# Kernel optimization log

Measured on AMD Instinct MI355X. Metric: run time of the kernel, lower is better.

The kernel has to match this reference:

```python
import jax, jax.numpy as jnp
import numpy as np

R = 0.8      # jet radius used to normalize pairwise distances
BETA = 1.0   # EMD angular exponent (matches beta=1.0 in emd()/emd_loss default)


def setup_inputs() -> dict:
    key = jax.random.key(0)
    k1, k2, k3, k4 = jax.random.split(key, 4)
    Ni, Nj, D = 6144, 6144, 2   # event points, shape-sample points, (eta, phi)
    M, K = 1024, 256            # batched simplex projection: rows x components
    y_i = jax.random.normal(k1, (Ni, D), dtype=jnp.float32)
    y_j = jax.random.normal(k2, (Nj, D), dtype=jnp.float32)
    x = jax.random.uniform(k3, (Ni, Nj), dtype=jnp.float32)
    x_ij = x / jnp.sum(x)       # transport plan normalized to unit total mass
    f = jax.random.normal(k4, (M, K), dtype=jnp.float32)
    return {"y_i": y_i, "y_j": y_j, "x_ij": x_ij, "f": f}


def _activate(f):
    # Euclidean projection of each row of f onto the probability simplex
    # (sort descending -> running threshold -> relu shift), as in activate().
    m, n = f.shape
    u = jnp.sort(f, axis=1)[:, ::-1]                                   # [m, n] descending
    v = (jnp.cumsum(u, axis=1) - 1.0) / jnp.arange(1, n + 1, dtype=f.dtype)
    rho = jnp.sum((u > v).astype(jnp.int32), axis=1) - 1               # [m]
    w = jnp.take_along_axis(v, rho[:, None], axis=1)                   # [m, 1]
    return jax.nn.relu(f - w)


def _emd_loss(y_i, y_j, x_ij):
    # theta_ij = sum_d | ((y_i - y_j) / R)^beta |  ; loss = sum theta_ij * x_ij
    diff = (y_i[:, None, :] - y_j[None, :, :]) / R                     # [Ni, Nj, D]
    theta = jnp.sum(jnp.abs(diff ** BETA), axis=-1)                    # [Ni, Nj]
    return jnp.sum(theta * x_ij)


def reference(y_i, y_j, x_ij, f):
    loss = _emd_loss(y_i, y_j, x_ij)   # scalar EMD-style transport loss
    z_proj = _activate(f)              # [M, K] simplex-projected weights
    return (loss, z_proj)
```

## Files before the change

### kernel.cpp

```cpp
#include <hip/hip_runtime.h>

#define NI 6144
#define NJ 6144
#define M_ROWS 1024
#define K_COLS 256
#define ROWS_PER_BLOCK 6
#define EMD_BLOCKS (NI / ROWS_PER_BLOCK)

__global__ __launch_bounds__(256) void emd_partial_kernel(
    const float* __restrict__ y_i, const float* __restrict__ y_j,
    const float* __restrict__ x, float* __restrict__ partial) {
  __shared__ float4 yjs[NJ / 2];
  const float4* yj4 = (const float4*)y_j;
  for (int t = threadIdx.x; t < NJ / 2; t += 256) yjs[t] = yj4[t];
  __syncthreads();

  float acc = 0.0f;
  const int row0 = blockIdx.x * ROWS_PER_BLOCK;
  for (int r = 0; r < ROWS_PER_BLOCK; ++r) {
    const int i = row0 + r;
    const float yi0 = y_i[2 * i];
    const float yi1 = y_i[2 * i + 1];
    const float4* xrow = (const float4*)(x + (size_t)i * NJ);
#pragma unroll
    for (int t = 0; t < NJ / 4 / 256; ++t) {
      const int idx = threadIdx.x + t * 256;
      const float4 xv = xrow[idx];
      const float4 ya = yjs[2 * idx];
      const float4 yb = yjs[2 * idx + 1];
      acc += xv.x * (fabsf(yi0 - ya.x) + fabsf(yi1 - ya.y));
      acc += xv.y * (fabsf(yi0 - ya.z) + fabsf(yi1 - ya.w));
      acc += xv.z * (fabsf(yi0 - yb.x) + fabsf(yi1 - yb.y));
      acc += xv.w * (fabsf(yi0 - yb.z) + fabsf(yi1 - yb.w));
    }
  }

  for (int off = 32; off > 0; off >>= 1) acc += __shfl_down(acc, off, 64);
  __shared__ float wsum[4];
  const int lane = threadIdx.x & 63;
  const int wid = threadIdx.x >> 6;
  if (lane == 0) wsum[wid] = acc;
  __syncthreads();
  if (threadIdx.x == 0)
    partial[blockIdx.x] = wsum[0] + wsum[1] + wsum[2] + wsum[3];
}

__global__ __launch_bounds__(256) void simplex_and_finish_kernel(
    const float* __restrict__ f, const float* __restrict__ partial,
    float* __restrict__ out) {
  const int tid = threadIdx.x;

  if (blockIdx.x == M_ROWS) {
    float acc = partial[tid] + partial[tid + 256] + partial[tid + 512] +
                partial[tid + 768];
    for (int off = 32; off > 0; off >>= 1) acc += __shfl_down(acc, off, 64);
    __shared__ float wsum[4];
    const int lane = tid & 63;
    const int wid = tid >> 6;
    if (lane == 0) wsum[wid] = acc;
    __syncthreads();
    if (tid == 0)
      out[0] = (wsum[0] + wsum[1] + wsum[2] + wsum[3]) * 1.25f;
    return;
  }

  const int row = blockIdx.x;
  const float fv = f[row * K_COLS + tid];

  __shared__ float s[K_COLS];
  __shared__ float c0[K_COLS];
  __shared__ float c1[K_COLS];
  __shared__ float vbuf[K_COLS];

  s[tid] = fv;
  __syncthreads();

  for (int k = 2; k <= K_COLS; k <<= 1) {
    for (int j = k >> 1; j > 0; j >>= 1) {
      const int ixj = tid ^ j;
      if (ixj > tid) {
        const float a = s[tid];
        const float b = s[ixj];
        const bool asc = ((tid & k) == 0);
        if ((a > b) == asc) {
          s[tid] = b;
          s[ixj] = a;
        }
      }
      __syncthreads();
    }
  }

  const float u = s[K_COLS - 1 - tid];
  c0[tid] = u;
  __syncthreads();
  float* src = c0;
  float* dst = c1;
  for (int off = 1; off < K_COLS; off <<= 1) {
    float v = src[tid];
    if (tid >= off) v += src[tid - off];
    dst[tid] = v;
    __syncthreads();
    float* tmp = src; src = dst; dst = tmp;
  }
  const float cs = src[tid];
  const float vt = (cs - 1.0f) / (float)(tid + 1);
  vbuf[tid] = vt;
  const int cnt = __syncthreads_count(u > vt);
  const float w = vbuf[cnt - 1];

  out[1 + row * K_COLS + tid] = fmaxf(fv - w, 0.0f);
}

extern "C" void kernel_launch(void* const* d_in, const int* in_sizes, int n_in,
                              void* d_out, int out_size, void* d_ws,
                              size_t ws_size, hipStream_t stream) {
  const float* y_i = (const float*)d_in[0];
  const float* y_j = (const float*)d_in[1];
  const float* x   = (const float*)d_in[2];
  const float* f   = (const float*)d_in[3];
  float* out = (float*)d_out;
  float* partial = (float*)d_ws;

  emd_partial_kernel<<<EMD_BLOCKS, 256, 0, stream>>>(y_i, y_j, x, partial);
  simplex_and_finish_kernel<<<M_ROWS + 1, 256, 0, stream>>>(f, partial, out);
}
```

Before: 235.2 us.

## Split y_j into component arrays, interleave rows per block, shuffle-based sort and scan

The EMD kernel now stores the eta and phi components of y_j in separate shared arrays. It processes 8 rows per block with the row loop inside the column loop, so each y_j load from shared memory is reused across all rows and several independent x loads are in flight at once. The simplex kernel replaces its shared-memory bitonic sort and Hillis-Steele scan with wavefront shuffles, using shared memory only for the cross-wave stages. This cuts barriers and LDS traffic but raises register pressure. The finishing reduction is adjusted to the new count of 768 partials.

```diff
diff --git a/kernel.cpp b/kernel.cpp
--- a/kernel.cpp
+++ b/kernel.cpp
@@ -4,34 +4,48 @@
 #define NJ 6144
 #define M_ROWS 1024
 #define K_COLS 256
-#define ROWS_PER_BLOCK 6
+#define ROWS_PER_BLOCK 8
 #define EMD_BLOCKS (NI / ROWS_PER_BLOCK)
 
 __global__ __launch_bounds__(256) void emd_partial_kernel(
     const float* __restrict__ y_i, const float* __restrict__ y_j,
     const float* __restrict__ x, float* __restrict__ partial) {
-  __shared__ float4 yjs[NJ / 2];
-  const float4* yj4 = (const float4*)y_j;
-  for (int t = threadIdx.x; t < NJ / 2; t += 256) yjs[t] = yj4[t];
+  __shared__ float4 yj0v[NJ / 4];
+  __shared__ float4 yj1v[NJ / 4];
+  {
+    const float4* yj4 = (const float4*)y_j;
+    float* s0 = (float*)yj0v;
+    float* s1 = (float*)yj1v;
+    for (int t = threadIdx.x; t < NJ / 2; t += 256) {
+      const float4 v = yj4[t];
+      s0[2 * t]     = v.x;  s1[2 * t]     = v.y;
+      s0[2 * t + 1] = v.z;  s1[2 * t + 1] = v.w;
+    }
+  }
   __syncthreads();
 
+  const int row0 = blockIdx.x * ROWS_PER_BLOCK;
+  float yi0[ROWS_PER_BLOCK], yi1[ROWS_PER_BLOCK];
+#pragma unroll
+  for (int r = 0; r < ROWS_PER_BLOCK; ++r) {
+    yi0[r] = y_i[2 * (row0 + r)];
+    yi1[r] = y_i[2 * (row0 + r) + 1];
+  }
+
   float acc = 0.0f;
-  const int row0 = blockIdx.x * ROWS_PER_BLOCK;
-  for (int r = 0; r < ROWS_PER_BLOCK; ++r) {
-    const int i = row0 + r;
-    const float yi0 = y_i[2 * i];
-    const float yi1 = y_i[2 * i + 1];
-    const float4* xrow = (const float4*)(x + (size_t)i * NJ);
 #pragma unroll
-    for (int t = 0; t < NJ / 4 / 256; ++t) {
-      const int idx = threadIdx.x + t * 256;
-      const float4 xv = xrow[idx];
-      const float4 ya = yjs[2 * idx];
-      const float4 yb = yjs[2 * idx + 1];
-      acc += xv.x * (fabsf(yi0 - ya.x) + fabsf(yi1 - ya.y));
-      acc += xv.y * (fabsf(yi0 - ya.z) + fabsf(yi1 - ya.w));
-      acc += xv.z * (fabsf(yi0 - yb.x) + fabsf(yi1 - yb.y));
-      acc += xv.w * (fabsf(yi0 - yb.z) + fabsf(yi1 - yb.w));
+  for (int t = 0; t < NJ / 4 / 256; ++t) {
+    const int idx = threadIdx.x + t * 256;
+    const float4 ya = yj0v[idx];
+    const float4 yb = yj1v[idx];
+#pragma unroll
+    for (int r = 0; r < ROWS_PER_BLOCK; ++r) {
+      const float4 xv =
+          ((const float4*)(x + (size_t)(row0 + r) * NJ))[idx];
+      acc += xv.x * (fabsf(yi0[r] - ya.x) + fabsf(yi1[r] - yb.x));
+      acc += xv.y * (fabsf(yi0[r] - ya.y) + fabsf(yi1[r] - yb.y));
+      acc += xv.z * (fabsf(yi0[r] - ya.z) + fabsf(yi1[r] - yb.z));
+      acc += xv.w * (fabsf(yi0[r] - ya.w) + fabsf(yi1[r] - yb.w));
     }
   }
 
@@ -49,65 +63,81 @@
     const float* __restrict__ f, const float* __restrict__ partial,
     float* __restrict__ out) {
   const int tid = threadIdx.x;
+  const int lane = tid & 63;
+  const int wid = tid >> 6;
+
+  __shared__ float s[K_COLS];
+  __shared__ float wpre[4];
 
   if (blockIdx.x == M_ROWS) {
-    float acc = partial[tid] + partial[tid + 256] + partial[tid + 512] +
-                partial[tid + 768];
+    float acc = partial[tid] + partial[tid + 256] + partial[tid + 512];
     for (int off = 32; off > 0; off >>= 1) acc += __shfl_down(acc, off, 64);
-    __shared__ float wsum[4];
-    const int lane = tid & 63;
-    const int wid = tid >> 6;
-    if (lane == 0) wsum[wid] = acc;
+    if (lane == 0) wpre[wid] = acc;
     __syncthreads();
     if (tid == 0)
-      out[0] = (wsum[0] + wsum[1] + wsum[2] + wsum[3]) * 1.25f;
+      out[0] = (wpre[0] + wpre[1] + wpre[2] + wpre[3]) * 1.25f;
     return;
   }
 
   const int row = blockIdx.x;
   const float fv = f[row * K_COLS + tid];
 
-  __shared__ float s[K_COLS];
-  __shared__ float c0[K_COLS];
-  __shared__ float c1[K_COLS];
-  __shared__ float vbuf[K_COLS];
-
-  s[tid] = fv;
-  __syncthreads();
-
-  for (int k = 2; k <= K_COLS; k <<= 1) {
+  float x = fv;
+#pragma unroll
+  for (int k = 2; k <= 64; k <<= 1) {
+#pragma unroll
     for (int j = k >> 1; j > 0; j >>= 1) {
-      const int ixj = tid ^ j;
-      if (ixj > tid) {
-        const float a = s[tid];
-        const float b = s[ixj];
-        const bool asc = ((tid & k) == 0);
-        if ((a > b) == asc) {
-          s[tid] = b;
-          s[ixj] = a;
-        }
-      }
-      __syncthreads();
+      const float pv = __shfl_xor(x, j, 64);
+      const bool up = ((tid & k) == 0);
+      const bool lower = ((tid & j) == 0);
+      x = (up == lower) ? fmaxf(x, pv) : fminf(x, pv);
+    }
+  }
+  {
+    s[tid] = x; __syncthreads();
+    const float pv = s[tid ^ 64]; __syncthreads();
+    const bool up = ((tid & 128) == 0);
+    x = (up == ((tid & 64) == 0)) ? fmaxf(x, pv) : fminf(x, pv);
+#pragma unroll
+    for (int j = 32; j > 0; j >>= 1) {
+      const float pv2 = __shfl_xor(x, j, 64);
+      x = (up == ((tid & j) == 0)) ? fmaxf(x, pv2) : fminf(x, pv2);
+    }
+  }
+  {
+    s[tid] = x; __syncthreads();
+    float pv = s[tid ^ 128]; __syncthreads();
+    x = ((tid & 128) == 0) ? fmaxf(x, pv) : fminf(x, pv);
+    s[tid] = x; __syncthreads();
+    pv = s[tid ^ 64]; __syncthreads();
+    x = ((tid & 64) == 0) ? fmaxf(x, pv) : fminf(x, pv);
+#pragma unroll
+    for (int j = 32; j > 0; j >>= 1) {
+      const float pv2 = __shfl_xor(x, j, 64);
+      x = ((tid & j) == 0) ? fmaxf(x, pv2) : fminf(x, pv2);
     }
   }
 
-  const float u = s[K_COLS - 1 - tid];
-  c0[tid] = u;
+  const float u = x;
+
+  float cs = u;
+#pragma unroll
+  for (int off = 1; off < 64; off <<= 1) {
+    const float t = __shfl_up(cs, off, 64);
+    if (lane >= off) cs += t;
+  }
+  if (lane == 63) wpre[wid] = cs;
   __syncthreads();
-  float* src = c0;
-  float* dst = c1;
-  for (int off = 1; off < K_COLS; off <<= 1) {
-    float v = src[tid];
-    if (tid >= off) v += src[tid - off];
-    dst[tid] = v;
-    __syncthreads();
-    float* tmp = src; src = dst; dst = tmp;
-  }
-  const float cs = src[tid];
+  float base = 0.0f;
+#pragma unroll
+  for (int w = 0; w < 4; ++w)
+    if (w < wid) base += wpre[w];
+  cs += base;
+
   const float vt = (cs - 1.0f) / (float)(tid + 1);
-  vbuf[tid] = vt;
+  s[tid] = vt;
   const int cnt = __syncthreads_count(u > vt);
-  const float w = vbuf[cnt - 1];
+  const float w = s[cnt - 1];
 
   out[1 + row * K_COLS + tid] = fmaxf(fv - w, 0.0f);
 }
```

Result: faster. 228.3 us (-2.9%).
